# Kernel tuning notes

Hardware: AMD Instinct MI355X
Metric: run time of the kernel (lower is better)

Reference implementation:

```python
import jax, jax.numpy as jnp
import numpy as np

B, T, N, D = 16, 12, 512, 128
H, DH = 4, 32            # heads, per-head dim (out_dim = H*DH = 128)
E = 4096                  # edges in the static road graph
NEG_SLOPE = 0.2
LN_EPS = 1e-5


def setup_inputs() -> dict:
    key = jax.random.key(0)
    ks = jax.random.split(key, 9)
    x = jax.random.normal(ks[0], (B, T, N, D), dtype=jnp.float32)
    edge_index = jax.random.randint(ks[1], (2, E), 0, N, dtype=jnp.int64)
    edge_weight = jax.random.uniform(ks[2], (E,), dtype=jnp.float32)
    # GAT parameters (dropout in eval mode -> identity)
    W = jax.random.normal(ks[3], (D, H * DH), dtype=jnp.float32) * (1.0 / np.sqrt(D))
    att_src = jax.random.normal(ks[4], (H, DH), dtype=jnp.float32) * 0.1
    att_dst = jax.random.normal(ks[5], (H, DH), dtype=jnp.float32) * 0.1
    bias = jnp.zeros((H * DH,), dtype=jnp.float32)
    ln_gamma = jnp.ones((H * DH,), dtype=jnp.float32)
    ln_beta = jnp.zeros((H * DH,), dtype=jnp.float32)
    return {"x": x, "edge_index": edge_index, "edge_weight": edge_weight,
            "W": W, "att_src": att_src, "att_dst": att_dst, "bias": bias,
            "ln_gamma": ln_gamma, "ln_beta": ln_beta}


def reference(x, edge_index, edge_weight, W, att_src, att_dst, bias, ln_gamma, ln_beta):
    b, t, n, din = x.shape
    bt = b * t
    h_heads, dh = att_src.shape
    src, dst = edge_index[0], edge_index[1]

    # project: [BT, N, H, DH]
    h = (x.reshape(bt, n, din) @ W).reshape(bt, n, h_heads, dh)

    # per-node attention scores, then gather to edges: [BT, E, H]
    s_src = jnp.einsum('bnhd,hd->bnh', h, att_src)
    s_dst = jnp.einsum('bnhd,hd->bnh', h, att_dst)
    e = jax.nn.leaky_relu(s_src[:, src] + s_dst[:, dst], NEG_SLOPE)
    e = e * edge_weight[None, :, None]  # edge_weight modulates attention logits

    # scatter-softmax over incoming edges per destination node
    m = jnp.full((bt, n, h_heads), -1e30, dtype=e.dtype).at[:, dst].max(e)
    ex = jnp.exp(e - m[:, dst])
    denom = jnp.zeros((bt, n, h_heads), dtype=e.dtype).at[:, dst].add(ex)
    alpha = ex / (denom[:, dst] + 1e-16)  # [BT, E, H]

    # weighted aggregation (scatter-add) of source features
    msg = alpha[..., None] * h[:, src]  # [BT, E, H, DH]
    agg = jnp.zeros((bt, n, h_heads, dh), dtype=h.dtype).at[:, dst].add(msg)

    out = agg.reshape(b, t, n, h_heads * dh) + bias

    # LayerNorm then ELU
    mu = out.mean(axis=-1, keepdims=True)
    var = out.var(axis=-1, keepdims=True)
    out = (out - mu) * jax.lax.rsqrt(var + LN_EPS) * ln_gamma + ln_beta
    return jnp.where(out > 0, out, jnp.expm1(out))
```

## Files before the change

### kernel.cpp

```cpp
#include <hip/hip_runtime.h>

#define BT    192
#define NNODE 512
#define DIM   128
#define NH    4
#define DH    32
#define NE    4096
#define NROWS (BT * NNODE)

typedef __attribute__((ext_vector_type(8))) short  short8b;
typedef __attribute__((ext_vector_type(4))) float  floatx4;
typedef __attribute__((ext_vector_type(8))) unsigned short ushort8;

__device__ inline unsigned short f2bf(float f) {
    unsigned int u = __float_as_uint(f);
    return (unsigned short)((u + 0x7FFFu + ((u >> 16) & 1u)) >> 16);
}
__device__ inline float bflo(unsigned int v) { return __uint_as_float(v << 16); }
__device__ inline float bfhi(unsigned int v) { return __uint_as_float(v & 0xFFFF0000u); }

__device__ inline short8b pack8(float4 a, float4 b) {
    short8b r;
    r[0] = (short)f2bf(a.x); r[1] = (short)f2bf(a.y);
    r[2] = (short)f2bf(a.z); r[3] = (short)f2bf(a.w);
    r[4] = (short)f2bf(b.x); r[5] = (short)f2bf(b.y);
    r[6] = (short)f2bf(b.z); r[7] = (short)f2bf(b.w);
    return r;
}

__global__ __launch_bounds__(512) void csr_build_k(
    const int* __restrict__ ei, const float* __restrict__ ew,
    const float* __restrict__ W,
    int* __restrict__ row_ptr, int* __restrict__ csr_src,
    float* __restrict__ csr_ew, unsigned short* __restrict__ wswz)
{
    __shared__ int dsts[NE];
    __shared__ int cnt[NNODE];
    __shared__ int scan[NNODE];
    int t = threadIdx.x;
    int b = blockIdx.x;

    if (b >= 64) {
        int j = (b - 64) * 512 + t;
        const float4* W4 = (const float4*)W;
        float4 wv = W4[j];
        int k = j >> 5, c4 = (j & 31) * 4;
        float vv[4] = { wv.x, wv.y, wv.z, wv.w };
#pragma unroll
        for (int e = 0; e < 4; ++e) {
            int col = c4 + e;
            int byte = col * 256 + ((2 * k) ^ ((col & 7) << 4));
            wswz[byte >> 1] = f2bf(vv[e]);
        }
        return;
    }

    for (int e = t; e < NE; e += 512) dsts[e] = ei[NE + e];
    cnt[t] = 0;
    __syncthreads();
    for (int e = t; e < NE; e += 512) atomicAdd(&cnt[dsts[e]], 1);
    __syncthreads();
    scan[t] = cnt[t];
    __syncthreads();
    for (int o = 1; o < NNODE; o <<= 1) {
        int v = (t >= o) ? scan[t - o] : 0;
        __syncthreads();
        scan[t] += v;
        __syncthreads();
    }
    if (b == 0) {
        if (t == 0) row_ptr[0] = 0;
        row_ptr[t + 1] = scan[t];
    }
    __syncthreads();

    int wave = t >> 6, lane = t & 63;
    int node = b * 8 + wave;
    int pos = scan[node] - cnt[node];
    for (int c = 0; c < NE; c += 64) {
        int e = c + lane;
        int d = dsts[e];
        unsigned long long mask = __ballot(d == node);
        if (d == node) {
            int ofs = __popcll(mask & ((1ull << lane) - 1ull));
            csr_src[pos + ofs] = ei[e];
            csr_ew[pos + ofs]  = ew[e];
        }
        pos += __popcll(mask);
    }
}

__global__ __launch_bounds__(256) void gemm_mfma_k(
    const float* __restrict__ x, const unsigned short* __restrict__ wswz,
    unsigned short* __restrict__ h)
{
    __shared__ __align__(16) char sm[64 * 132 * 4];
    int t = threadIdx.x;
    {
        const uint4* g = (const uint4*)wswz;
        uint4* ld = (uint4*)sm;
#pragma unroll
        for (int i = 0; i < 8; ++i) ld[t + i * 256] = g[t + i * 256];
    }
    int w = t >> 6, l = t & 63, lr = l & 15, lk = l >> 4;
    size_t base = (size_t)blockIdx.x * 128;
    const float* xA = x + (base + (size_t)w * 16 + lr) * DIM;
    const float* xB = xA + 64 * DIM;

    floatx4 accA[8], accB[8];
#pragma unroll
    for (int n = 0; n < 8; ++n) {
        accA[n] = (floatx4){0.f, 0.f, 0.f, 0.f};
        accB[n] = (floatx4){0.f, 0.f, 0.f, 0.f};
    }
    __syncthreads();

#pragma unroll
    for (int kk = 0; kk < 4; ++kk) {
        int k0 = kk * 32 + lk * 8;
        float4 a0 = *(const float4*)(xA + k0);
        float4 a1 = *(const float4*)(xA + k0 + 4);
        float4 b0 = *(const float4*)(xB + k0);
        float4 b1 = *(const float4*)(xB + k0 + 4);
        short8b av = pack8(a0, a1);
        short8b bv = pack8(b0, b1);
        int c = kk * 4 + lk;
#pragma unroll
        for (int n = 0; n < 8; ++n) {
            int col = n * 16 + lr;
            short8b bf = *(const short8b*)(sm + col * 256 + ((c ^ (col & 7)) << 4));
            accA[n] = __builtin_amdgcn_mfma_f32_16x16x32_bf16(av, bf, accA[n], 0, 0, 0);
            accB[n] = __builtin_amdgcn_mfma_f32_16x16x32_bf16(bv, bf, accB[n], 0, 0, 0);
        }
    }

    float* Ct = (float*)sm;
    unsigned short* hbase = h + base * DIM;

    __syncthreads();
#pragma unroll
    for (int n = 0; n < 8; ++n)
#pragma unroll
        for (int j = 0; j < 4; ++j)
            Ct[(w * 16 + lk * 4 + j) * 132 + n * 16 + lr] = accA[n][j];
    __syncthreads();
#pragma unroll
    for (int i = 0; i < 4; ++i) {
        int chunk = t + i * 256;
        int row = chunk >> 4, cc = chunk & 15;
        const float* cp = Ct + row * 132 + cc * 8;
        ushort8 v;
#pragma unroll
        for (int e = 0; e < 8; ++e) v[e] = f2bf(cp[e]);
        *(ushort8*)(hbase + row * DIM + cc * 8) = v;
    }

    __syncthreads();
#pragma unroll
    for (int n = 0; n < 8; ++n)
#pragma unroll
        for (int j = 0; j < 4; ++j)
            Ct[(w * 16 + lk * 4 + j) * 132 + n * 16 + lr] = accB[n][j];
    __syncthreads();
#pragma unroll
    for (int i = 0; i < 4; ++i) {
        int chunk = t + i * 256;
        int row = chunk >> 4, cc = chunk & 15;
        const float* cp = Ct + row * 132 + cc * 8;
        ushort8 v;
#pragma unroll
        for (int e = 0; e < 8; ++e) v[e] = f2bf(cp[e]);
        *(ushort8*)(hbase + (64 + row) * DIM + cc * 8) = v;
    }
}

__global__ __launch_bounds__(256) void attn_agg_k(
    const unsigned short* __restrict__ h,
    const float* __restrict__ att_src, const float* __restrict__ att_dst,
    const int* __restrict__ row_ptr, const int* __restrict__ csr_src,
    const float* __restrict__ csr_ew, unsigned short* __restrict__ agg)
{
    __shared__ unsigned int hs[NNODE * 17];
    __shared__ float ssrc[NNODE];
    __shared__ float sdst[NNODE];
    __shared__ float att_s[64];
    int t    = threadIdx.x;
    int head = blockIdx.x & 3;
    int bt   = blockIdx.x >> 2;

    const unsigned short* hbase = h + (size_t)bt * NNODE * DIM + head * DH;
    for (int idx = t; idx < NNODE * 4; idx += 256) {
        int node = idx >> 2, q = idx & 3;
        ushort8 v = *(const ushort8*)(hbase + (size_t)node * DIM + q * 8);
        const unsigned int* vi = (const unsigned int*)&v;
        unsigned int* p = hs + node * 17 + q * 4;
        p[0] = vi[0]; p[1] = vi[1]; p[2] = vi[2]; p[3] = vi[3];
    }
    if (t < 32)       att_s[t] = att_src[head * DH + t];
    else if (t < 64)  att_s[t] = att_dst[head * DH + (t - 32)];
    __syncthreads();

    for (int node = t; node < NNODE; node += 256) {
        const unsigned int* hp = hs + node * 17;
        float a = 0.f, b = 0.f;
#pragma unroll
        for (int j = 0; j < 16; ++j) {
            unsigned int v = hp[j];
            float lo = bflo(v), hi = bfhi(v);
            a = fmaf(lo, att_s[2*j], a);    a = fmaf(hi, att_s[2*j+1], a);
            b = fmaf(lo, att_s[32+2*j], b); b = fmaf(hi, att_s[32+2*j+1], b);
        }
        ssrc[node] = a;
        sdst[node] = b;
    }
    __syncthreads();

    for (int node = t; node < NNODE; node += 256) {
        int beg = row_ptr[node], end = row_ptr[node + 1];
        float sd = sdst[node];
        float denom = 0.f;
        float acc[DH];
#pragma unroll
        for (int d = 0; d < DH; ++d) acc[d] = 0.f;
        for (int e = beg; e < end; ++e) {
            int s = csr_src[e];
            float sc = ssrc[s] + sd;
            sc = (sc > 0.f) ? sc : 0.2f * sc;
            sc *= csr_ew[e];
            float p = __expf(sc);
            denom += p;
            const unsigned int* hp = hs + s * 17;
#pragma unroll
            for (int j = 0; j < 16; ++j) {
                unsigned int v = hp[j];
                acc[2*j]   = fmaf(p, bflo(v), acc[2*j]);
                acc[2*j+1] = fmaf(p, bfhi(v), acc[2*j+1]);
            }
        }
        float inv = 1.f / (denom + 1e-16f);
        unsigned short* op = agg + ((size_t)bt * NNODE + node) * DIM + head * DH;
#pragma unroll
        for (int c = 0; c < 4; ++c) {
            ushort8 v;
#pragma unroll
            for (int e = 0; e < 8; ++e) v[e] = f2bf(acc[c * 8 + e] * inv);
            *(ushort8*)(op + c * 8) = v;
        }
    }
}

__global__ __launch_bounds__(256) void ln_elu_k(
    const unsigned int* __restrict__ agg, float* __restrict__ out,
    const float* __restrict__ bias,
    const float* __restrict__ gamma, const float* __restrict__ beta)
{
    int lane = threadIdx.x & 63;
    int wave = threadIdx.x >> 6;
    size_t row = (size_t)blockIdx.x * 4 + wave;
    unsigned int v = agg[row * 64 + lane];
    float2 bb = *(const float2*)(bias + lane * 2);
    float vx = bflo(v) + bb.x;
    float vy = bfhi(v) + bb.y;
    float s  = vx + vy;
    float sq = fmaf(vx, vx, vy * vy);
#pragma unroll
    for (int o = 32; o > 0; o >>= 1) {
        s  += __shfl_xor(s,  o, 64);
        sq += __shfl_xor(sq, o, 64);
    }
    float mean = s * (1.f / 128.f);
    float var  = sq * (1.f / 128.f) - mean * mean;
    float rstd = rsqrtf(var + 1e-5f);
    float2 g  = *(const float2*)(gamma + lane * 2);
    float2 be = *(const float2*)(beta  + lane * 2);
    float y0 = (vx - mean) * rstd * g.x + be.x;
    float y1 = (vy - mean) * rstd * g.y + be.y;
    y0 = (y0 > 0.f) ? y0 : expm1f(y0);
    y1 = (y1 > 0.f) ? y1 : expm1f(y1);
    float2 o2 = { y0, y1 };
    *(float2*)(out + row * DIM + lane * 2) = o2;
}

extern "C" void kernel_launch(void* const* d_in, const int* in_sizes, int n_in,
                              void* d_out, int out_size, void* d_ws, size_t ws_size,
                              hipStream_t stream)
{
    const float* x     = (const float*)d_in[0];
    const int*   ei    = (const int*)  d_in[1];
    const float* ew    = (const float*)d_in[2];
    const float* W     = (const float*)d_in[3];
    const float* asrc  = (const float*)d_in[4];
    const float* adst  = (const float*)d_in[5];
    const float* bias  = (const float*)d_in[6];
    const float* gamma = (const float*)d_in[7];
    const float* beta  = (const float*)d_in[8];
    float* out = (float*)d_out;

    char* ws = (char*)d_ws;
    unsigned short* h = (unsigned short*)ws;
    size_t off = (size_t)NROWS * DIM * sizeof(unsigned short);
    unsigned short* agg = (unsigned short*)(ws + off);
    off += (size_t)NROWS * DIM * sizeof(unsigned short);
    unsigned short* wswz = (unsigned short*)(ws + off);
    off += (size_t)DIM * DIM * sizeof(unsigned short);
    int* row_ptr = (int*)(ws + off);
    off += (((NNODE + 1) * sizeof(int)) + 15) & ~(size_t)15;
    int* csr_src = (int*)(ws + off);
    off += (size_t)NE * sizeof(int);
    float* csr_ew = (float*)(ws + off);
    off += (size_t)NE * sizeof(float);

    csr_build_k<<<72, 512, 0, stream>>>(ei, ew, W, row_ptr, csr_src, csr_ew, wswz);
    gemm_mfma_k<<<NROWS / 128, 256, 0, stream>>>(x, wswz, h);
    attn_agg_k<<<BT * NH, 256, 0, stream>>>(h, asrc, adst, row_ptr, csr_src, csr_ew, agg);
    ln_elu_k<<<NROWS / 4, 256, 0, stream>>>((const unsigned int*)agg, out, bias, gamma, beta);
}
```

Baseline: 78.42 us.

## Fuse attention scores into GEMM epilogue and merge aggregation with LayerNorm-ELU

The GEMM epilogue now computes per-node source and destination attention scores from the fp32 accumulators and writes them to workspace. The separate attention-aggregation and LayerNorm/ELU kernels are replaced by one kernel where each thread handles one node across all four heads. That thread gathers neighbour h rows from global memory, normalizes, then applies LayerNorm and ELU in registers. This removes the bf16 agg intermediate round trip and one launch, and drops LDS staging of h. In exchange it needs 128 accumulator registers per thread and uses uncoalesced per-thread row gathers.

```diff
diff --git a/kernel.cpp b/kernel.cpp
--- a/kernel.cpp
+++ b/kernel.cpp
@@ -92,10 +92,15 @@
 
 __global__ __launch_bounds__(256) void gemm_mfma_k(
     const float* __restrict__ x, const unsigned short* __restrict__ wswz,
-    unsigned short* __restrict__ h)
+    const float* __restrict__ att_src, const float* __restrict__ att_dst,
+    unsigned short* __restrict__ h, float* __restrict__ ssg,
+    float* __restrict__ sdg)
 {
     __shared__ __align__(16) char sm[64 * 132 * 4];
+    __shared__ float att_f[256];
     int t = threadIdx.x;
+    if (t < 128) att_f[t] = att_src[(t & 3) * 32 + (t >> 2)];
+    else         att_f[t] = att_dst[(t & 3) * 32 + ((t - 128) >> 2)];
     {
         const uint4* g = (const uint4*)wswz;
         uint4* ld = (uint4*)sm;
@@ -136,6 +141,7 @@
 
     float* Ct = (float*)sm;
     unsigned short* hbase = h + base * DIM;
+    int sr = t >> 2, sq = t & 3;
 
     __syncthreads();
 #pragma unroll
@@ -154,6 +160,25 @@
         for (int e = 0; e < 8; ++e) v[e] = f2bf(cp[e]);
         *(ushort8*)(hbase + row * DIM + cc * 8) = v;
     }
+    {
+        const float* cp = Ct + sr * 132 + sq * 32;
+        float ps = 0.f, pd = 0.f;
+#pragma unroll
+        for (int j = 0; j < 32; j += 4) {
+            float4 cv = *(const float4*)(cp + j);
+            ps = fmaf(cv.x, att_f[(j+0)*4 + sq], ps);
+            ps = fmaf(cv.y, att_f[(j+1)*4 + sq], ps);
+            ps = fmaf(cv.z, att_f[(j+2)*4 + sq], ps);
+            ps = fmaf(cv.w, att_f[(j+3)*4 + sq], ps);
+            pd = fmaf(cv.x, att_f[128 + (j+0)*4 + sq], pd);
+            pd = fmaf(cv.y, att_f[128 + (j+1)*4 + sq], pd);
+            pd = fmaf(cv.z, att_f[128 + (j+2)*4 + sq], pd);
+            pd = fmaf(cv.w, att_f[128 + (j+3)*4 + sq], pd);
+        }
+        size_t grow = base + sr;
+        ssg[grow * 4 + sq] = ps;
+        sdg[grow * 4 + sq] = pd;
+    }
 
     __syncthreads();
 #pragma unroll
@@ -172,113 +197,117 @@
         for (int e = 0; e < 8; ++e) v[e] = f2bf(cp[e]);
         *(ushort8*)(hbase + (64 + row) * DIM + cc * 8) = v;
     }
-}
-
-__global__ __launch_bounds__(256) void attn_agg_k(
+    {
+        const float* cp = Ct + sr * 132 + sq * 32;
+        float ps = 0.f, pd = 0.f;
+#pragma unroll
+        for (int j = 0; j < 32; j += 4) {
+            float4 cv = *(const float4*)(cp + j);
+            ps = fmaf(cv.x, att_f[(j+0)*4 + sq], ps);
+            ps = fmaf(cv.y, att_f[(j+1)*4 + sq], ps);
+            ps = fmaf(cv.z, att_f[(j+2)*4 + sq], ps);
+            ps = fmaf(cv.w, att_f[(j+3)*4 + sq], ps);
+            pd = fmaf(cv.x, att_f[128 + (j+0)*4 + sq], pd);
+            pd = fmaf(cv.y, att_f[128 + (j+1)*4 + sq], pd);
+            pd = fmaf(cv.z, att_f[128 + (j+2)*4 + sq], pd);
+            pd = fmaf(cv.w, att_f[128 + (j+3)*4 + sq], pd);
+        }
+        size_t grow = base + 64 + sr;
+        ssg[grow * 4 + sq] = ps;
+        sdg[grow * 4 + sq] = pd;
+    }
+}
+
+__global__ __launch_bounds__(256) void agg_ln_k(
     const unsigned short* __restrict__ h,
-    const float* __restrict__ att_src, const float* __restrict__ att_dst,
+    const float* __restrict__ ssg, const float* __restrict__ sdg,
     const int* __restrict__ row_ptr, const int* __restrict__ csr_src,
-    const float* __restrict__ csr_ew, unsigned short* __restrict__ agg)
+    const float* __restrict__ csr_ew,
+    const float* __restrict__ bias, const float* __restrict__ gamma,
+    const float* __restrict__ beta, float* __restrict__ out)
 {
-    __shared__ unsigned int hs[NNODE * 17];
-    __shared__ float ssrc[NNODE];
-    __shared__ float sdst[NNODE];
-    __shared__ float att_s[64];
-    int t    = threadIdx.x;
-    int head = blockIdx.x & 3;
-    int bt   = blockIdx.x >> 2;
-
-    const unsigned short* hbase = h + (size_t)bt * NNODE * DIM + head * DH;
-    for (int idx = t; idx < NNODE * 4; idx += 256) {
-        int node = idx >> 2, q = idx & 3;
-        ushort8 v = *(const ushort8*)(hbase + (size_t)node * DIM + q * 8);
-        const unsigned int* vi = (const unsigned int*)&v;
-        unsigned int* p = hs + node * 17 + q * 4;
-        p[0] = vi[0]; p[1] = vi[1]; p[2] = vi[2]; p[3] = vi[3];
-    }
-    if (t < 32)       att_s[t] = att_src[head * DH + t];
-    else if (t < 64)  att_s[t] = att_dst[head * DH + (t - 32)];
-    __syncthreads();
-
-    for (int node = t; node < NNODE; node += 256) {
-        const unsigned int* hp = hs + node * 17;
-        float a = 0.f, b = 0.f;
-#pragma unroll
-        for (int j = 0; j < 16; ++j) {
-            unsigned int v = hp[j];
-            float lo = bflo(v), hi = bfhi(v);
-            a = fmaf(lo, att_s[2*j], a);    a = fmaf(hi, att_s[2*j+1], a);
-            b = fmaf(lo, att_s[32+2*j], b); b = fmaf(hi, att_s[32+2*j+1], b);
-        }
-        ssrc[node] = a;
-        sdst[node] = b;
-    }
-    __syncthreads();
-
-    for (int node = t; node < NNODE; node += 256) {
-        int beg = row_ptr[node], end = row_ptr[node + 1];
-        float sd = sdst[node];
-        float denom = 0.f;
-        float acc[DH];
-#pragma unroll
-        for (int d = 0; d < DH; ++d) acc[d] = 0.f;
-        for (int e = beg; e < end; ++e) {
-            int s = csr_src[e];
-            float sc = ssrc[s] + sd;
-            sc = (sc > 0.f) ? sc : 0.2f * sc;
-            sc *= csr_ew[e];
-            float p = __expf(sc);
-            denom += p;
-            const unsigned int* hp = hs + s * 17;
-#pragma unroll
-            for (int j = 0; j < 16; ++j) {
-                unsigned int v = hp[j];
-                acc[2*j]   = fmaf(p, bflo(v), acc[2*j]);
-                acc[2*j+1] = fmaf(p, bfhi(v), acc[2*j+1]);
+    __shared__ float bgb[384];
+    int t = threadIdx.x;
+    for (int i = t; i < 384; i += 256)
+        bgb[i] = (i < 128) ? bias[i] : (i < 256) ? gamma[i - 128] : beta[i - 256];
+    __syncthreads();
+
+    int gid  = blockIdx.x * 256 + t;
+    int node = gid & (NNODE - 1);
+    int bt   = gid >> 9;
+    const unsigned short* hb  = h   + (size_t)bt * NNODE * DIM;
+    const float*          ssb = ssg + (size_t)bt * NNODE * 4;
+    float4 sd = *(const float4*)(sdg + (size_t)gid * 4);
+    int beg = row_ptr[node], end = row_ptr[node + 1];
+
+    float acc[DIM];
+#pragma unroll
+    for (int d = 0; d < DIM; ++d) acc[d] = 0.f;
+    float den0 = 0.f, den1 = 0.f, den2 = 0.f, den3 = 0.f;
+
+    for (int e = beg; e < end; ++e) {
+        int s   = csr_src[e];
+        float w = csr_ew[e];
+        float4 ss = *(const float4*)(ssb + s * 4);
+        float e0 = ss.x + sd.x; e0 = (e0 > 0.f) ? e0 : 0.2f * e0;
+        float e1 = ss.y + sd.y; e1 = (e1 > 0.f) ? e1 : 0.2f * e1;
+        float e2 = ss.z + sd.z; e2 = (e2 > 0.f) ? e2 : 0.2f * e2;
+        float e3 = ss.w + sd.w; e3 = (e3 > 0.f) ? e3 : 0.2f * e3;
+        float p0 = __expf(e0 * w), p1 = __expf(e1 * w);
+        float p2 = __expf(e2 * w), p3 = __expf(e3 * w);
+        den0 += p0; den1 += p1; den2 += p2; den3 += p3;
+        const uint4* hp = (const uint4*)(hb + (size_t)s * DIM);
+#pragma unroll
+        for (int q = 0; q < 4; ++q) {
+            float pq = (q == 0) ? p0 : (q == 1) ? p1 : (q == 2) ? p2 : p3;
+#pragma unroll
+            for (int i = 0; i < 4; ++i) {
+                uint4 v = hp[q * 4 + i];
+                int d0 = q * 32 + i * 8;
+                acc[d0+0] = fmaf(pq, bflo(v.x), acc[d0+0]);
+                acc[d0+1] = fmaf(pq, bfhi(v.x), acc[d0+1]);
+                acc[d0+2] = fmaf(pq, bflo(v.y), acc[d0+2]);
+                acc[d0+3] = fmaf(pq, bfhi(v.y), acc[d0+3]);
+                acc[d0+4] = fmaf(pq, bflo(v.z), acc[d0+4]);
+                acc[d0+5] = fmaf(pq, bfhi(v.z), acc[d0+5]);
+                acc[d0+6] = fmaf(pq, bflo(v.w), acc[d0+6]);
+                acc[d0+7] = fmaf(pq, bfhi(v.w), acc[d0+7]);
             }
         }
-        float inv = 1.f / (denom + 1e-16f);
-        unsigned short* op = agg + ((size_t)bt * NNODE + node) * DIM + head * DH;
-#pragma unroll
-        for (int c = 0; c < 4; ++c) {
-            ushort8 v;
-#pragma unroll
-            for (int e = 0; e < 8; ++e) v[e] = f2bf(acc[c * 8 + e] * inv);
-            *(ushort8*)(op + c * 8) = v;
-        }
-    }
-}
-
-__global__ __launch_bounds__(256) void ln_elu_k(
-    const unsigned int* __restrict__ agg, float* __restrict__ out,
-    const float* __restrict__ bias,
-    const float* __restrict__ gamma, const float* __restrict__ beta)
-{
-    int lane = threadIdx.x & 63;
-    int wave = threadIdx.x >> 6;
-    size_t row = (size_t)blockIdx.x * 4 + wave;
-    unsigned int v = agg[row * 64 + lane];
-    float2 bb = *(const float2*)(bias + lane * 2);
-    float vx = bflo(v) + bb.x;
-    float vy = bfhi(v) + bb.y;
-    float s  = vx + vy;
-    float sq = fmaf(vx, vx, vy * vy);
-#pragma unroll
-    for (int o = 32; o > 0; o >>= 1) {
-        s  += __shfl_xor(s,  o, 64);
-        sq += __shfl_xor(sq, o, 64);
-    }
-    float mean = s * (1.f / 128.f);
-    float var  = sq * (1.f / 128.f) - mean * mean;
+    }
+
+#pragma unroll
+    for (int q = 0; q < 4; ++q) {
+        float dq  = (q == 0) ? den0 : (q == 1) ? den1 : (q == 2) ? den2 : den3;
+        float inv = 1.f / (dq + 1e-16f);
+#pragma unroll
+        for (int j = 0; j < 32; ++j) {
+            int d = q * 32 + j;
+            acc[d] = fmaf(acc[d], inv, bgb[d]);
+        }
+    }
+
+    float s1 = 0.f, s2 = 0.f;
+#pragma unroll
+    for (int d = 0; d < DIM; ++d) { s1 += acc[d]; s2 = fmaf(acc[d], acc[d], s2); }
+    float mean = s1 * (1.f / 128.f);
+    float var  = s2 * (1.f / 128.f) - mean * mean;
     float rstd = rsqrtf(var + 1e-5f);
-    float2 g  = *(const float2*)(gamma + lane * 2);
-    float2 be = *(const float2*)(beta  + lane * 2);
-    float y0 = (vx - mean) * rstd * g.x + be.x;
-    float y1 = (vy - mean) * rstd * g.y + be.y;
-    y0 = (y0 > 0.f) ? y0 : expm1f(y0);
-    y1 = (y1 > 0.f) ? y1 : expm1f(y1);
-    float2 o2 = { y0, y1 };
-    *(float2*)(out + row * DIM + lane * 2) = o2;
+
+    float* op = out + (size_t)gid * DIM;
+#pragma unroll
+    for (int d = 0; d < DIM; d += 4) {
+        float4 o4;
+        float y0 = (acc[d+0] - mean) * rstd * bgb[128 + d+0] + bgb[256 + d+0];
+        float y1 = (acc[d+1] - mean) * rstd * bgb[128 + d+1] + bgb[256 + d+1];
+        float y2 = (acc[d+2] - mean) * rstd * bgb[128 + d+2] + bgb[256 + d+2];
+        float y3 = (acc[d+3] - mean) * rstd * bgb[128 + d+3] + bgb[256 + d+3];
+        o4.x = (y0 > 0.f) ? y0 : expm1f(y0);
+        o4.y = (y1 > 0.f) ? y1 : expm1f(y1);
+        o4.z = (y2 > 0.f) ? y2 : expm1f(y2);
+        o4.w = (y3 > 0.f) ? y3 : expm1f(y3);
+        *(float4*)(op + d) = o4;
+    }
 }
 
 extern "C" void kernel_launch(void* const* d_in, const int* in_sizes, int n_in,
@@ -299,10 +328,12 @@
     char* ws = (char*)d_ws;
     unsigned short* h = (unsigned short*)ws;
     size_t off = (size_t)NROWS * DIM * sizeof(unsigned short);
-    unsigned short* agg = (unsigned short*)(ws + off);
-    off += (size_t)NROWS * DIM * sizeof(unsigned short);
     unsigned short* wswz = (unsigned short*)(ws + off);
     off += (size_t)DIM * DIM * sizeof(unsigned short);
+    float* ssg = (float*)(ws + off);
+    off += (size_t)NROWS * NH * sizeof(float);
+    float* sdg = (float*)(ws + off);
+    off += (size_t)NROWS * NH * sizeof(float);
     int* row_ptr = (int*)(ws + off);
     off += (((NNODE + 1) * sizeof(int)) + 15) & ~(size_t)15;
     int* csr_src = (int*)(ws + off);
@@ -311,7 +342,7 @@
     off += (size_t)NE * sizeof(float);
 
     csr_build_k<<<72, 512, 0, stream>>>(ei, ew, W, row_ptr, csr_src, csr_ew, wswz);
-    gemm_mfma_k<<<NROWS / 128, 256, 0, stream>>>(x, wswz, h);
-    attn_agg_k<<<BT * NH, 256, 0, stream>>>(h, asrc, adst, row_ptr, csr_src, csr_ew, agg);
-    ln_elu_k<<<NROWS / 4, 256, 0, stream>>>((const unsigned int*)agg, out, bias, gamma, beta);
-}
+    gemm_mfma_k<<<NROWS / 128, 256, 0, stream>>>(x, wswz, asrc, adst, h, ssg, sdg);
+    agg_ln_k<<<NROWS / 256, 256, 0, stream>>>(h, ssg, sdg, row_ptr, csr_src, csr_ew,
+                                              bias, gamma, beta, out);
+}
```

Result: slower. 98.33 us (+25.4%).
